# Kernel optimization log

Measured on AMD Instinct MI355X. Metric: run time of the kernel, lower is better.

Reference implementation:

```python
import jax, jax.numpy as jnp
import numpy as np

EPS = 1e-5
COMMITMENT_WEIGHT = 1.0


def setup_inputs() -> dict:
    key = jax.random.key(0)
    k1, k2 = jax.random.split(key)
    x = jax.random.normal(k1, (4, 4096, 128), dtype=jnp.float32)
    codebook = jax.random.normal(k2, (8192, 128), dtype=jnp.float32)
    return {"x": x, "codebook": codebook}


def _layernorm(x):
    # LayerNorm over last dim, elementwise_affine=False, eps=1e-5
    mu = jnp.mean(x, axis=-1, keepdims=True)
    var = jnp.mean(jnp.square(x - mu), axis=-1, keepdims=True)
    return (x - mu) * jax.lax.rsqrt(var + EPS)


def reference(x, codebook):
    b, n, d = x.shape
    xn = _layernorm(x)                      # [b, n, d]
    flat = xn.reshape(b * n, d)             # [bn, d]
    x2 = jnp.sum(flat * flat, axis=-1, keepdims=True)          # [bn, 1]
    e2 = jnp.sum(codebook * codebook, axis=-1)                  # [K]
    dots = jnp.einsum('nd,kd->nk', flat, codebook)              # [bn, K]
    distances = x2 - 2.0 * dots + e2[None, :]                   # [bn, K]
    embed_ind = jnp.argmin(distances, axis=-1)                  # [bn]
    quantize = codebook[embed_ind].reshape(b, n, d)             # gather
    embed_ind = embed_ind.reshape(b, n)
    loss = jnp.mean(jnp.square(quantize - xn)) * COMMITMENT_WEIGHT
    # straight-through
    quantize_st = xn + jax.lax.stop_gradient(quantize - xn)
    return (quantize_st, embed_ind, loss)
```

## Files before the change

kernel.cpp:

```cpp
#include <hip/hip_runtime.h>
#include <hip/hip_fp16.h>
#include <math.h>

typedef _Float16 half8  __attribute__((ext_vector_type(8)));
typedef _Float16 half2v __attribute__((ext_vector_type(2)));
typedef float   floatx4 __attribute__((ext_vector_type(4)));

#define ROWS   16384
#define DIM    128
#define KCODES 8192
#define NSPLIT 8
#define KSPLIT (KCODES / NSPLIT)
#define NGROUP (KSPLIT / 16)
#define MTILE  256
#define DELTA  0.5f

__device__ __forceinline__ void async_copy16(const void* src, void* dst_lds) {
  __builtin_amdgcn_global_load_lds((const __attribute__((address_space(1))) void*)src,
                                   (__attribute__((address_space(3))) void*)dst_lds,
                                   16, 0, 0);
}

__global__ __launch_bounds__(256) void prep_kernel(
    const float* __restrict__ cb, const float* __restrict__ x,
    _Float16* __restrict__ ehg, float* __restrict__ e2g,
    _Float16* __restrict__ xnh, float* __restrict__ out_loss)
{
  int tid = threadIdx.x;
  int L = tid & 63;
  int bx = blockIdx.x;
  if (bx == 0 && tid == 0) *out_loss = 0.f;
  if (bx < KCODES / 4) {
    int row = bx * 4 + (tid >> 6);
    float2 v = ((const float2*)(cb + (size_t)row * DIM))[L];
    float s2 = v.x * v.x + v.y * v.y;
    #pragma unroll
    for (int m = 1; m < 64; m <<= 1) s2 += __shfl_xor(s2, m);
    if (L == 0) e2g[row] = -0.5f * s2;
    half2v hi = {(_Float16)v.x, (_Float16)v.y};
    ((half2v*)(ehg + (size_t)row * DIM))[L] = hi;
  } else {
    int row = (bx - KCODES / 4) * 4 + (tid >> 6);
    float2 xv = ((const float2*)(x + (size_t)row * DIM))[L];
    float s = xv.x + xv.y;
    #pragma unroll
    for (int m = 1; m < 64; m <<= 1) s += __shfl_xor(s, m);
    float mu = s * (1.0f / 128.0f);
    float dx = xv.x - mu, dy = xv.y - mu;
    float s2 = dx * dx + dy * dy;
    #pragma unroll
    for (int m = 1; m < 64; m <<= 1) s2 += __shfl_xor(s2, m);
    float rstd = 1.0f / sqrtf(s2 * (1.0f / 128.0f) + 1e-5f);
    half2v hv = {(_Float16)(dx * rstd), (_Float16)(dy * rstd)};
    ((half2v*)(xnh + (size_t)row * DIM))[L] = hv;
  }
}

__global__ __launch_bounds__(256, 2) void argmin_kernel(
    const _Float16* __restrict__ xnh, const _Float16* __restrict__ ehg,
    const float* __restrict__ e2g,
    float* __restrict__ b1p, int* __restrict__ i1p,
    float* __restrict__ b2p, int* __restrict__ i2p)
{
  __shared__ _Float16 ebuf[4][3][16][128];
  __shared__ float e2l[KSPLIT];

  int tid = threadIdx.x;
  int w = tid >> 6, L = tid & 63, c = L & 15, q = L >> 4;
  int bx = blockIdx.x;
  int mt = bx & (ROWS / MTILE - 1);
  int ns = bx >> 6;
  int rowbase = mt * MTILE + w * 64;
  int code0 = ns * KSPLIT;

  half8 ah[4][4];
  #pragma unroll
  for (int g = 0; g < 4; ++g) {
    const _Float16* xr = xnh + (size_t)(rowbase + g * 16 + c) * DIM;
    #pragma unroll
    for (int ks = 0; ks < 4; ++ks)
      ah[g][ks] = *(const half8*)(xr + ks * 32 + q * 8);
  }

  {
    float4 v = ((const float4*)(e2g + code0))[tid];
    float4 o = {256.f + v.x, 256.f + v.y, 256.f + v.z, 256.f + v.w};
    ((float4*)e2l)[tid] = o;
  }
  __syncthreads();

  _Float16* wbase = &ebuf[w][0][0][0];
  auto stage = [&](int g, int ring) {
    int cbase = code0 + g * 16;
    _Float16* lb = wbase + ring * (16 * 128);
    #pragma unroll
    for (int it = 0; it < 4; ++it) {
      int cid = it * 64 + L;
      int n   = cid >> 4;
      int kcs = cid & 15;
      int kc  = kcs ^ (n & 7);
      async_copy16(ehg + (size_t)(cbase + n) * DIM + kc * 8, lb + cid * 8);
    }
  };
  stage(0, 0); stage(1, 1); stage(2, 2);

  unsigned k1[4][4], k2[4][4];
  #pragma unroll
  for (int g = 0; g < 4; ++g)
    #pragma unroll
    for (int r = 0; r < 4; ++r) { k1[g][r] = 0u; k2[g][r] = 0u; }

  for (int g = 0; g < NGROUP; ++g) {
    if (g + 2 < NGROUP)      asm volatile("s_waitcnt vmcnt(8)" ::: "memory");
    else if (g + 1 < NGROUP) asm volatile("s_waitcnt vmcnt(4)" ::: "memory");
    else                     asm volatile("s_waitcnt vmcnt(0)" ::: "memory");

    const _Float16* buf = wbase + (g % 3) * (16 * 128);
    float e2v = e2l[(size_t)g * 16 + c];
    half8 bh[4];
    #pragma unroll
    for (int ks = 0; ks < 4; ++ks)
      bh[ks] = *(const half8*)(buf + (size_t)c * 128 + ((ks * 4 + q) ^ (c & 7)) * 8);

    unsigned gp = (unsigned)g;
    #pragma unroll
    for (int gg = 0; gg < 4; ++gg) {
      floatx4 acc = {e2v, e2v, e2v, e2v};
      #pragma unroll
      for (int ks = 0; ks < 4; ++ks)
        acc = __builtin_amdgcn_mfma_f32_16x16x32_f16(ah[gg][ks], bh[ks], acc, 0, 0, 0);
      #pragma unroll
      for (int r = 0; r < 4; ++r) {
        unsigned kk = (__float_as_uint(acc[r]) & 0xFFFFFFC0u) | gp;
        unsigned tt = kk < k1[gg][r] ? kk : k1[gg][r];
        k1[gg][r] = kk > k1[gg][r] ? kk : k1[gg][r];
        k2[gg][r] = tt > k2[gg][r] ? tt : k2[gg][r];
      }
    }
    asm volatile("s_waitcnt lgkmcnt(0)" ::: "memory");
    if (g + 3 < NGROUP) stage(g + 3, g % 3);
  }

  #pragma unroll
  for (int gg = 0; gg < 4; ++gg)
    #pragma unroll
    for (int r = 0; r < 4; ++r) {
      float s1 = __uint_as_float(k1[gg][r] & 0xFFFFFFC0u) - 256.f;
      float s2 = __uint_as_float(k2[gg][r] & 0xFFFFFFC0u) - 256.f;
      int   j1 = code0 + (int)(k1[gg][r] & 63u) * 16 + c;
      int   j2 = code0 + (int)(k2[gg][r] & 63u) * 16 + c;
      #pragma unroll
      for (int m = 1; m < 16; m <<= 1) {
        float o1 = __shfl_xor(s1, m); int oj1 = __shfl_xor(j1, m);
        float o2 = __shfl_xor(s2, m); int oj2 = __shfl_xor(j2, m);
        if (o1 > s1) {
          bool t = (s1 >= o2);
          s2 = t ? s1 : o2;  j2 = t ? j1 : oj2;
          s1 = o1; j1 = oj1;
        } else {
          bool t = (o1 >= s2);
          s2 = t ? o1 : s2;  j2 = t ? oj1 : j2;
        }
      }
      if (c == 0) {
        int row = rowbase + gg * 16 + q * 4 + r;
        b1p[(size_t)row * NSPLIT + ns] = s1; i1p[(size_t)row * NSPLIT + ns] = j1;
        b2p[(size_t)row * NSPLIT + ns] = s2; i2p[(size_t)row * NSPLIT + ns] = j2;
      }
    }
}

__global__ __launch_bounds__(256) void gather_loss_kernel(
    const float* __restrict__ x, const float* __restrict__ cb,
    const float* __restrict__ e2g,
    const float* __restrict__ b1p, const int* __restrict__ i1p,
    const float* __restrict__ b2p, const int* __restrict__ i2p,
    float* __restrict__ out_q, float* __restrict__ out_ind,
    float* __restrict__ out_loss)
{
  __shared__ float lsum[4];
  int tid = threadIdx.x;
  int L = tid & 63;
  int w = tid >> 6;
  int row = blockIdx.x * 4 + w;

  int k  = L & 15;
  int qd = L >> 4;

  int ci = 0; float cv = -3.4e38f;
  if (L < 8)       { ci = i1p[(size_t)row * NSPLIT + L];       cv = b1p[(size_t)row * NSPLIT + L]; }
  else if (L < 16) { ci = i2p[(size_t)row * NSPLIT + (L - 8)]; cv = b2p[(size_t)row * NSPLIT + (L - 8)]; }
  int   idxk = __shfl(ci, k);
  float tvk  = __shfl(cv, k);

  float tmax = tvk;
  #pragma unroll
  for (int m = 1; m < 16; m <<= 1) tmax = fmaxf(tmax, __shfl_xor(tmax, m));
  bool keep = tvk >= tmax - DELTA;

  float2 xv = ((const float2*)(x + (size_t)row * DIM))[L];
  float s = xv.x + xv.y;
  #pragma unroll
  for (int m = 1; m < 64; m <<= 1) s += __shfl_xor(s, m);
  float mu = s * (1.0f / 128.0f);
  float dx = xv.x - mu, dy = xv.y - mu;
  float s2 = dx * dx + dy * dy;
  #pragma unroll
  for (int m = 1; m < 64; m <<= 1) s2 += __shfl_xor(s2, m);
  float rstd = 1.0f / sqrtf(s2 * (1.0f / 128.0f) + 1e-5f);

  float p = 0.f;
  if (keep) {
    const float4* xr4 = (const float4*)(x  + (size_t)row  * DIM);
    const float4* er4 = (const float4*)(cb + (size_t)idxk * DIM);
    #pragma unroll
    for (int j = 0; j < 8; ++j) {
      float4 a = xr4[qd * 8 + j];
      float4 e = er4[qd * 8 + j];
      p += (a.x - mu) * e.x + (a.y - mu) * e.y + (a.z - mu) * e.z + (a.w - mu) * e.w;
    }
    p *= rstd;
  }
  p += __shfl_xor(p, 16);
  p += __shfl_xor(p, 32);
  float t = keep ? p + e2g[idxk] : -3.4e38f;

  int bi = idxk;
  #pragma unroll
  for (int m = 1; m < 16; m <<= 1) {
    float ot = __shfl_xor(t, m);
    int   oi = __shfl_xor(bi, m);
    if (ot > t || (ot == t && oi < bi)) { t = ot; bi = oi; }
  }

  float2 qv = ((const float2*)(cb + (size_t)bi * DIM))[L];
  ((float2*)out_q)[(size_t)row * 64 + L] = qv;
  float xn0 = dx * rstd, xn1 = dy * rstd;
  float e0 = qv.x - xn0, e1 = qv.y - xn1;
  float le = e0 * e0 + e1 * e1;
  #pragma unroll
  for (int m = 1; m < 64; m <<= 1) le += __shfl_xor(le, m);
  if (L == 0) {
    lsum[w] = le;
    out_ind[row] = (float)bi;
  }
  __syncthreads();
  if (tid == 0)
    atomicAdd(out_loss, (lsum[0] + lsum[1] + lsum[2] + lsum[3]) * (1.0f / ((float)ROWS * DIM)));
}

extern "C" void kernel_launch(void* const* d_in, const int* in_sizes, int n_in,
                              void* d_out, int out_size, void* d_ws, size_t ws_size,
                              hipStream_t stream)
{
  const float* x  = (const float*)d_in[0];
  const float* cb = (const float*)d_in[1];

  char* ws = (char*)d_ws;
  _Float16* ehg = (_Float16*)(ws + 0);
  float*    e2g = (float*)   (ws + 2097152);
  float*    b1p = (float*)   (ws + 2129920);
  int*      i1p = (int*)     (ws + 2654208);
  float*    b2p = (float*)   (ws + 3178496);
  int*      i2p = (int*)     (ws + 3702784);

  float* out_q    = (float*)d_out;
  float* out_ind  = out_q + (size_t)ROWS * DIM;
  float* out_loss = out_ind + ROWS;

  _Float16* xnh = (_Float16*)out_q;

  prep_kernel<<<KCODES / 4 + ROWS / 4, 256, 0, stream>>>(cb, x, ehg, e2g, xnh, out_loss);
  argmin_kernel<<<(ROWS / MTILE) * NSPLIT, 256, 0, stream>>>(xnh, ehg, e2g, b1p, i1p, b2p, i2p);
  gather_loss_kernel<<<ROWS / 4, 256, 0, stream>>>(x, cb, e2g, b1p, i1p, b2p, i2p, out_q, out_ind, out_loss);
}
```

Measured before the change: 182.5 us.

## Double codebook split, shrink LDS ring, skip rescoring for unique candidates

```diff
diff --git a/kernel.cpp b/kernel.cpp
--- a/kernel.cpp
+++ b/kernel.cpp
@@ -9,11 +9,11 @@
 #define ROWS   16384
 #define DIM    128
 #define KCODES 8192
-#define NSPLIT 8
+#define NSPLIT 16
 #define KSPLIT (KCODES / NSPLIT)
 #define NGROUP (KSPLIT / 16)
 #define MTILE  256
-#define DELTA  0.5f
+#define THR    0.3f
 
 __device__ __forceinline__ void async_copy16(const void* src, void* dst_lds) {
   __builtin_amdgcn_global_load_lds((const __attribute__((address_space(1))) void*)src,
@@ -62,7 +62,7 @@
     float* __restrict__ b1p, int* __restrict__ i1p,
     float* __restrict__ b2p, int* __restrict__ i2p)
 {
-  __shared__ _Float16 ebuf[4][3][16][128];
+  __shared__ _Float16 ebuf[4][2][16][128];
   __shared__ float e2l[KSPLIT];
 
   int tid = threadIdx.x;
@@ -82,27 +82,32 @@
       ah[g][ks] = *(const half8*)(xr + ks * 32 + q * 8);
   }
 
-  {
+  if (tid < KSPLIT / 4) {
     float4 v = ((const float4*)(e2g + code0))[tid];
     float4 o = {256.f + v.x, 256.f + v.y, 256.f + v.z, 256.f + v.w};
     ((float4*)e2l)[tid] = o;
   }
+
+  const _Float16* gsrc[4];
+  _Float16*       ldst[2][4];
+  #pragma unroll
+  for (int it = 0; it < 4; ++it) {
+    int cid = it * 64 + L;
+    int n   = cid >> 4;
+    int kcs = cid & 15;
+    int kc  = kcs ^ (n & 7);
+    gsrc[it]    = ehg + (size_t)(code0 + n) * DIM + kc * 8;
+    ldst[0][it] = &ebuf[w][0][0][0] + cid * 8;
+    ldst[1][it] = &ebuf[w][1][0][0] + cid * 8;
+  }
   __syncthreads();
 
-  _Float16* wbase = &ebuf[w][0][0][0];
   auto stage = [&](int g, int ring) {
-    int cbase = code0 + g * 16;
-    _Float16* lb = wbase + ring * (16 * 128);
-    #pragma unroll
-    for (int it = 0; it < 4; ++it) {
-      int cid = it * 64 + L;
-      int n   = cid >> 4;
-      int kcs = cid & 15;
-      int kc  = kcs ^ (n & 7);
-      async_copy16(ehg + (size_t)(cbase + n) * DIM + kc * 8, lb + cid * 8);
-    }
+    #pragma unroll
+    for (int it = 0; it < 4; ++it)
+      async_copy16(gsrc[it] + (size_t)g * 16 * DIM, ldst[ring][it]);
   };
-  stage(0, 0); stage(1, 1); stage(2, 2);
+  stage(0, 0); stage(1, 1);
 
   unsigned k1[4][4], k2[4][4];
   #pragma unroll
@@ -111,11 +116,10 @@
     for (int r = 0; r < 4; ++r) { k1[g][r] = 0u; k2[g][r] = 0u; }
 
   for (int g = 0; g < NGROUP; ++g) {
-    if (g + 2 < NGROUP)      asm volatile("s_waitcnt vmcnt(8)" ::: "memory");
-    else if (g + 1 < NGROUP) asm volatile("s_waitcnt vmcnt(4)" ::: "memory");
-    else                     asm volatile("s_waitcnt vmcnt(0)" ::: "memory");
-
-    const _Float16* buf = wbase + (g % 3) * (16 * 128);
+    if (g + 1 < NGROUP) asm volatile("s_waitcnt vmcnt(4)" ::: "memory");
+    else                asm volatile("s_waitcnt vmcnt(0)" ::: "memory");
+
+    const _Float16* buf = &ebuf[w][g & 1][0][0];
     float e2v = e2l[(size_t)g * 16 + c];
     half8 bh[4];
     #pragma unroll
@@ -137,8 +141,10 @@
         k2[gg][r] = tt > k2[gg][r] ? tt : k2[gg][r];
       }
     }
-    asm volatile("s_waitcnt lgkmcnt(0)" ::: "memory");
-    if (g + 3 < NGROUP) stage(g + 3, g % 3);
+    if (g + 2 < NGROUP) {
+      asm volatile("s_waitcnt lgkmcnt(0)" ::: "memory");
+      stage(g + 2, g & 1);
+    }
   }
 
   #pragma unroll
@@ -184,19 +190,20 @@
   int w = tid >> 6;
   int row = blockIdx.x * 4 + w;
 
-  int k  = L & 15;
-  int qd = L >> 4;
+  int k  = L & 31;
+  int qd = L >> 5;
 
   int ci = 0; float cv = -3.4e38f;
-  if (L < 8)       { ci = i1p[(size_t)row * NSPLIT + L];       cv = b1p[(size_t)row * NSPLIT + L]; }
-  else if (L < 16) { ci = i2p[(size_t)row * NSPLIT + (L - 8)]; cv = b2p[(size_t)row * NSPLIT + (L - 8)]; }
+  if (L < 16)      { ci = i1p[(size_t)row * NSPLIT + L];        cv = b1p[(size_t)row * NSPLIT + L]; }
+  else if (L < 32) { ci = i2p[(size_t)row * NSPLIT + (L - 16)]; cv = b2p[(size_t)row * NSPLIT + (L - 16)]; }
   int   idxk = __shfl(ci, k);
   float tvk  = __shfl(cv, k);
 
   float tmax = tvk;
   #pragma unroll
-  for (int m = 1; m < 16; m <<= 1) tmax = fmaxf(tmax, __shfl_xor(tmax, m));
-  bool keep = tvk >= tmax - DELTA;
+  for (int m = 1; m < 32; m <<= 1) tmax = fmaxf(tmax, __shfl_xor(tmax, m));
+  bool keep = tvk >= tmax - THR;
+  unsigned long long mb = __ballot(keep);
 
   float2 xv = ((const float2*)(x + (size_t)row * DIM))[L];
   float s = xv.x + xv.y;
@@ -209,28 +216,32 @@
   for (int m = 1; m < 64; m <<= 1) s2 += __shfl_xor(s2, m);
   float rstd = 1.0f / sqrtf(s2 * (1.0f / 128.0f) + 1e-5f);
 
-  float p = 0.f;
-  if (keep) {
-    const float4* xr4 = (const float4*)(x  + (size_t)row  * DIM);
-    const float4* er4 = (const float4*)(cb + (size_t)idxk * DIM);
-    #pragma unroll
-    for (int j = 0; j < 8; ++j) {
-      float4 a = xr4[qd * 8 + j];
-      float4 e = er4[qd * 8 + j];
-      p += (a.x - mu) * e.x + (a.y - mu) * e.y + (a.z - mu) * e.z + (a.w - mu) * e.w;
-    }
-    p *= rstd;
-  }
-  p += __shfl_xor(p, 16);
-  p += __shfl_xor(p, 32);
-  float t = keep ? p + e2g[idxk] : -3.4e38f;
-
-  int bi = idxk;
-  #pragma unroll
-  for (int m = 1; m < 16; m <<= 1) {
-    float ot = __shfl_xor(t, m);
-    int   oi = __shfl_xor(bi, m);
-    if (ot > t || (ot == t && oi < bi)) { t = ot; bi = oi; }
+  int bi;
+  if (__popcll(mb) == 2) {
+    int lsel = (int)__ffsll(mb) - 1;
+    bi = __shfl(idxk, lsel);
+  } else {
+    float p = 0.f;
+    if (keep) {
+      const float4* xr4 = (const float4*)(x  + (size_t)row  * DIM);
+      const float4* er4 = (const float4*)(cb + (size_t)idxk * DIM);
+      #pragma unroll
+      for (int j = 0; j < 16; ++j) {
+        float4 a = xr4[qd * 16 + j];
+        float4 e = er4[qd * 16 + j];
+        p += (a.x - mu) * e.x + (a.y - mu) * e.y + (a.z - mu) * e.z + (a.w - mu) * e.w;
+      }
+      p *= rstd;
+    }
+    p += __shfl_xor(p, 32);
+    float t = keep ? p + e2g[idxk] : -3.4e38f;
+    bi = idxk;
+    #pragma unroll
+    for (int m = 1; m < 32; m <<= 1) {
+      float ot = __shfl_xor(t, m);
+      int   oi = __shfl_xor(bi, m);
+      if (ot > t || (ot == t && oi < bi)) { t = ot; bi = oi; }
+    }
   }
 
   float2 qv = ((const float2*)(cb + (size_t)bi * DIM))[L];
@@ -260,9 +271,9 @@
   _Float16* ehg = (_Float16*)(ws + 0);
   float*    e2g = (float*)   (ws + 2097152);
   float*    b1p = (float*)   (ws + 2129920);
-  int*      i1p = (int*)     (ws + 2654208);
-  float*    b2p = (float*)   (ws + 3178496);
-  int*      i2p = (int*)     (ws + 3702784);
+  int*      i1p = (int*)     (ws + 3178496);
+  float*    b2p = (float*)   (ws + 4227072);
+  int*      i2p = (int*)     (ws + 5275648);
 
   float* out_q    = (float*)d_out;
   float* out_ind  = out_q + (size_t)ROWS * DIM;
```

Result: no change. 180.5 us (-1.1%).
